# Performance work log

Hardware: AMD Instinct MI355X
Metric: run time of the kernel (lower is better)

## Reference

```python
import jax, jax.numpy as jnp
import numpy as np

N_MEL = 80


def _bce_with_logits(x, t):
    # mean over all elements, numerically stable
    return jnp.mean(jnp.maximum(x, 0.0) - x * t + jnp.log1p(jnp.exp(-jnp.abs(x))))


def _spectral_mel_loss(pred, target):
    w = np.ones(N_MEL, dtype=np.float32)
    w[N_MEL // 4: 3 * N_MEL // 4] *= 1.5
    w[3 * N_MEL // 4:] *= 0.8
    w = jnp.asarray(w)[None, :, None]
    weighted_mse = jnp.mean((pred * w - target * w) ** 2)
    l1 = jnp.mean(jnp.abs(pred - target))
    dp = pred[:, :, 1:] - pred[:, :, :-1]
    dt = target[:, :, 1:] - target[:, :, :-1]
    spectral = jnp.mean((dp - dt) ** 2)
    return weighted_mse + 0.3 * l1 + 0.2 * spectral


def _perceptual_loss(pred, target):
    fw = jnp.exp(-jnp.arange(N_MEL, dtype=jnp.float32) / 20.0)[None, :, None]
    weighted = ((pred - target) ** 2) * fw
    l1 = jnp.mean(jnp.abs(pred - target))
    return jnp.mean(weighted) + 0.5 * l1


def _style_loss(pred, target):
    mean_loss = jnp.mean((jnp.mean(pred, axis=2) - jnp.mean(target, axis=2)) ** 2)
    # torch.var defaults to unbiased (ddof=1)
    var_loss = jnp.mean((jnp.var(pred, axis=2, ddof=1) - jnp.var(target, axis=2, ddof=1)) ** 2)
    c, t = pred.shape[1], pred.shape[2]
    gram_p = jnp.einsum('bct,bdt->bcd', pred, pred) / (c * t)
    gram_t = jnp.einsum('bct,bdt->bcd', target, target) / (c * t)
    gram_loss = jnp.mean((gram_p - gram_t) ** 2)
    return mean_loss + var_loss + 0.5 * gram_loss


def _monotonic_loss(att):
    # att: [B, mel_len, text_len]; vectorized form of the per-step violation loop
    b, mel_len, _ = att.shape
    peaks = jnp.argmax(att, axis=2).astype(jnp.float32)  # [B, mel_len]
    viol = jnp.maximum(peaks[:, :-1] - peaks[:, 1:], 0.0)
    return jnp.sum(viol) / (b * mel_len)


def setup_inputs() -> dict:
    key = jax.random.key(0)
    ks = jax.random.split(key, 6)
    B, C, T, L = 64, N_MEL, 2000, 200
    return {
        'mel_out': jax.random.normal(ks[0], (B, C, T), jnp.float32),
        'mel_out_postnet': jax.random.normal(ks[1], (B, C, T), jnp.float32),
        'mel_target': jax.random.normal(ks[2], (B, C, T), jnp.float32),
        'gate_out': jax.random.normal(ks[3], (B, T), jnp.float32),
        'gate_target': jax.random.uniform(ks[4], (B, T), jnp.float32),
        'attention_weights': jax.random.uniform(ks[5], (B, T, L), jnp.float32),
    }


def reference(mel_out, mel_out_postnet, mel_target, gate_out, gate_target, attention_weights):
    # loss weights (hparams defaults); guide_loss omitted (method truncated in source)
    mel_w, gate_w, spec_w, perc_w, style_w, mono_w = 1.0, 1.0, 0.3, 0.2, 0.1, 0.1
    gate_inner_w = 1.3  # AdaptiveGateLoss initial_weight

    mel_loss = jnp.mean((mel_out - mel_target) ** 2) + jnp.mean((mel_out_postnet - mel_target) ** 2)
    gate_loss = gate_inner_w * _bce_with_logits(gate_out.reshape(-1, 1), gate_target.reshape(-1, 1))
    spectral = _spectral_mel_loss(mel_out_postnet, mel_target)
    perceptual = _perceptual_loss(mel_out_postnet, mel_target)
    style = _style_loss(mel_out_postnet, mel_target)
    mono = _monotonic_loss(attention_weights)

    total = (mel_w * mel_loss + gate_w * gate_loss + spec_w * spectral
             + perc_w * perceptual + style_w * style + mono_w * mono)
    return total
```

## Files before the change

kernel.cpp:

```cpp
#include <hip/hip_runtime.h>
#include <math.h>

#define N_MEL 80
#define B_    64
#define T_    2000
#define L_    200
#define ROWS   (B_*N_MEL)
#define NTOT   (B_*N_MEL*T_)
#define GATE_N (B_*T_)
#define ATT_ROWS (B_*T_)
#define AV_ROWS 64
#define NVIOL  (ATT_ROWS/AV_ROWS)

#define G_MELROW 5120
#define G_GRAM   512
#define G_ARGV   NVIOL
#define G_GATE   64

#define WS_ROWPART 0
#define WS_M8      (WS_ROWPART + ROWS*8)
#define WS_GATEP   (WS_M8 + 8*64*6400)
#define WS_VIOLP   (WS_GATEP + 64)
#define WS_GFP     (WS_VIOLP + NVIOL)

typedef __attribute__((ext_vector_type(8)))  short bf16x8;
typedef __attribute__((ext_vector_type(16))) float f32x16;
typedef unsigned short ush;

__device__ __forceinline__ float blockReduceSum256(float v) {
    __shared__ float red[4];
    #pragma unroll
    for (int off = 32; off; off >>= 1) v += __shfl_down(v, off, 64);
    int lane = threadIdx.x & 63, w = threadIdx.x >> 6;
    if (lane == 0) red[w] = v;
    __syncthreads();
    if (threadIdx.x == 0) v = red[0] + red[1] + red[2] + red[3];
    return v;
}

__device__ __forceinline__ unsigned short f2bf(float f) {
    unsigned u = __float_as_uint(f);
    u = (u + 0x7fffu + ((u >> 16) & 1u)) >> 16;
    return (unsigned short)u;
}

__device__ __forceinline__ void scan_sub(const float* __restrict__ rowp, int q,
                                         float& bOut, int& pOut) {
    const float4* rp = (const float4*)rowp;
    float bx=-1.f, by=-1.f, bz=-1.f, bw=-1.f;
    int jx=0, jy=0, jz=0, jw=0;
    const int n = (q < 2) ? 13 : 12;
    #pragma unroll
    for (int i = 0; i < 13; i++) {
        if (i < n) {
            int j = q + 4*i;
            float4 v = rp[j];
            if (v.x > bx) { bx = v.x; jx = j; }
            if (v.y > by) { by = v.y; jy = j; }
            if (v.z > bz) { bz = v.z; jz = j; }
            if (v.w > bw) { bw = v.w; jw = j; }
        }
    }
    float b = bx; int p = 4*jx;
    if (by > b || (by == b && 4*jy+1 < p)) { b = by; p = 4*jy+1; }
    if (bz > b || (bz == b && 4*jz+2 < p)) { b = bz; p = 4*jz+2; }
    if (bw > b || (bw == b && 4*jw+3 < p)) { b = bw; p = 4*jw+3; }
    bOut = b; pOut = p;
}

__device__ __forceinline__ void merge4(float& b, int& p) {
    #pragma unroll
    for (int m = 1; m <= 2; m <<= 1) {
        float ob = __shfl_xor(b, m, 64);
        int   op = __shfl_xor(p, m, 64);
        if (ob > b || (ob == b && op < p)) { b = ob; p = op; }
    }
}

__global__ __launch_bounds__(256) void k_mega(const float* __restrict__ mo,
                                              const float* __restrict__ mp,
                                              const float* __restrict__ mt,
                                              const float* __restrict__ gx,
                                              const float* __restrict__ gt,
                                              const float* __restrict__ att,
                                              float* __restrict__ ws) {
    __shared__ alignas(16) unsigned char smem[18432];
    const int bid = blockIdx.x;
    float* rowpart = ws + WS_ROWPART;
    float* M8      = ws + WS_M8;
    float* gatep   = ws + WS_GATEP;
    float* violp   = ws + WS_VIOLP;

    if (bid < G_MELROW) {
        const int row = bid;
        const long base = (long)row * T_;
        const float4* mo4 = (const float4*)(mo + base);
        const float4* mp4 = (const float4*)(mp + base);
        const float4* mt4 = (const float4*)(mt + base);

        float s1 = 0, s2 = 0, sl1 = 0, std_ = 0, sp = 0, sp2 = 0, st = 0, st2 = 0;
        for (int i = threadIdx.x; i < T_/4; i += 256) {
            float4 a = mo4[i], p = mp4[i], t = mt4[i];
            float e0 = a.x - t.x, e1 = a.y - t.y, e2 = a.z - t.z, e3 = a.w - t.w;
            s1 += e0*e0 + e1*e1 + e2*e2 + e3*e3;
            float d0 = p.x - t.x, d1 = p.y - t.y, d2 = p.z - t.z, d3 = p.w - t.w;
            s2 += d0*d0 + d1*d1 + d2*d2 + d3*d3;
            sl1 += fabsf(d0) + fabsf(d1) + fabsf(d2) + fabsf(d3);
            sp  += p.x + p.y + p.z + p.w;
            sp2 += p.x*p.x + p.y*p.y + p.z*p.z + p.w*p.w;
            st  += t.x + t.y + t.z + t.w;
            st2 += t.x*t.x + t.y*t.y + t.z*t.z + t.w*t.w;
            float q1 = d1 - d0, q2 = d2 - d1, q3 = d3 - d2;
            std_ += q1*q1 + q2*q2 + q3*q3;
            if (i > 0) {
                float dprev = mp[base + 4*i - 1] - mt[base + 4*i - 1];
                float q0 = d0 - dprev;
                std_ += q0*q0;
            }
        }

        float (*red)[8] = reinterpret_cast<float(*)[8]>(smem);
        float vals[8] = {s1, s2, sl1, std_, sp, sp2, st, st2};
        #pragma unroll
        for (int k = 0; k < 8; k++) {
            float v = vals[k];
            #pragma unroll
            for (int off = 32; off; off >>= 1) v += __shfl_down(v, off, 64);
            vals[k] = v;
        }
        int lane = threadIdx.x & 63, w = threadIdx.x >> 6;
        if (lane == 0) {
            #pragma unroll
            for (int k = 0; k < 8; k++) red[w][k] = vals[k];
        }
        __syncthreads();
        if (threadIdx.x == 0) {
            #pragma unroll
            for (int k = 0; k < 8; k++)
                rowpart[row*8 + k] = red[0][k] + red[1][k] + red[2][k] + red[3][k];
        }
        return;
    }

    if (bid < G_MELROW + G_GRAM) {
        const int gb = bid - G_MELROW;
        const int b  = gb >> 3;
        const int kc = gb & 7;
        const int k0 = kc * 256;
        const int NS = (kc < 7) ? 16 : 13;

        ush (*Dls)[96][24] = reinterpret_cast<ush(*)[96][24]>(smem);
        ush (*Sls)[96][24] = reinterpret_cast<ush(*)[96][24]>(smem + 9216);

        const int tid  = threadIdx.x;
        const bool act = (tid < 192);
        const int row  = tid >> 1;
        const int half = tid & 1;
        const int lane = tid & 63;
        const int wv   = tid >> 6;
        const long bbase = (long)b * (N_MEL * T_);
        const float* prow = mp + bbase + (long)(row < 80 ? row : 0) * T_ + k0 + half * 8;
        const float* trow = mt + bbase + (long)(row < 80 ? row : 0) * T_ + k0 + half * 8;
        const bool rv = act && (row < N_MEL);

        f32x16 acc0 = {}, acc1 = {}, acc2 = {};
        float4 pa0, pa1, ta0, ta1;

        auto loadreg = [&](int s) {
            if (rv) {
                pa0 = *(const float4*)(prow + s*16);
                pa1 = *(const float4*)(prow + s*16 + 4);
                ta0 = *(const float4*)(trow + s*16);
                ta1 = *(const float4*)(trow + s*16 + 4);
            } else {
                pa0 = pa1 = ta0 = ta1 = make_float4(0.f, 0.f, 0.f, 0.f);
            }
        };
        auto writelds = [&](int buf) {
            bf16x8 d, s;
            d[0]=f2bf(pa0.x-ta0.x); d[1]=f2bf(pa0.y-ta0.y); d[2]=f2bf(pa0.z-ta0.z); d[3]=f2bf(pa0.w-ta0.w);
            d[4]=f2bf(pa1.x-ta1.x); d[5]=f2bf(pa1.y-ta1.y); d[6]=f2bf(pa1.z-ta1.z); d[7]=f2bf(pa1.w-ta1.w);
            s[0]=f2bf(pa0.x+ta0.x); s[1]=f2bf(pa0.y+ta0.y); s[2]=f2bf(pa0.z+ta0.z); s[3]=f2bf(pa0.w+ta0.w);
            s[4]=f2bf(pa1.x+ta1.x); s[5]=f2bf(pa1.y+ta1.y); s[6]=f2bf(pa1.z+ta1.z); s[7]=f2bf(pa1.w+ta1.w);
            *(bf16x8*)&Dls[buf][row][half*8] = d;
            *(bf16x8*)&Sls[buf][row][half*8] = s;
        };

        if (act) { loadreg(0); writelds(0); }
        __syncthreads();

        const int frow = lane & 31;
        const int fkh  = lane >> 5;
        for (int s = 0; s < NS; s++) {
            const int cur = s & 1;
            if (act) {
                if (s + 1 < NS) loadreg(s + 1);
                bf16x8 af = *(const bf16x8*)&Dls[cur][wv*32 + frow][fkh*8];
                bf16x8 b0 = *(const bf16x8*)&Sls[cur][      frow][fkh*8];
                bf16x8 b1 = *(const bf16x8*)&Sls[cur][ 32 + frow][fkh*8];
                bf16x8 b2 = *(const bf16x8*)&Sls[cur][ 64 + frow][fkh*8];
                acc0 = __builtin_amdgcn_mfma_f32_32x32x16_bf16(af, b0, acc0, 0, 0, 0);
                acc1 = __builtin_amdgcn_mfma_f32_32x32x16_bf16(af, b1, acc1, 0, 0, 0);
                acc2 = __builtin_amdgcn_mfma_f32_32x32x16_bf16(af, b2, acc2, 0, 0, 0);
                if (s + 1 < NS) writelds((s + 1) & 1);
            }
            __syncthreads();
        }

        if (act) {
            float* Mb = M8 + ((long)(kc * B_ + b)) * 6400;
            #pragma unroll
            for (int r = 0; r < 16; r++) {
                int row32 = (r & 3) + 8 * (r >> 2) + 4 * (lane >> 5);
                int c = wv * 32 + row32;
                if (c < N_MEL) {
                    Mb[c*80 + frow]      = acc0[r];
                    Mb[c*80 + 32 + frow] = acc1[r];
                    if (frow < 16) Mb[c*80 + 64 + frow] = acc2[r];
                }
            }
        }
        return;
    }

    if (bid < G_MELROW + G_GRAM + G_ARGV) {
        const int ab = bid - (G_MELROW + G_GRAM);
        float* pk = reinterpret_cast<float*>(smem);
        const int g = threadIdx.x >> 2;
        const int q = threadIdx.x & 3;
        const int r0 = ab * AV_ROWS;
        const int r  = r0 + g;

        float b; int p;
        scan_sub(att + (long)r * L_, q, b, p);
        merge4(b, p);
        if (q == 0) pk[g] = (float)p;

        const int rb = r0 + AV_ROWS;
        const bool need_b = ((rb % T_) != 0) && (rb < ATT_ROWS);
        if (g == 0 && need_b) {
            float b2; int p2;
            scan_sub(att + (long)rb * L_, q, b2, p2);
            merge4(b2, p2);
            if (q == 0) pk[AV_ROWS] = (float)p2;
        }
        __syncthreads();

        float s = 0;
        if (threadIdx.x < AV_ROWS) {
            int rr = r0 + threadIdx.x;
            if (((rr + 1) % T_) != 0)
                s = fmaxf(pk[threadIdx.x] - pk[threadIdx.x + 1], 0.0f);
        }
        float tot = blockReduceSum256(s);
        if (threadIdx.x == 0) violp[ab] = tot;
        return;
    }

    {
        const int gb = bid - (G_MELROW + G_GRAM + G_ARGV);
        const float4* x4 = (const float4*)gx;
        const float4* t4 = (const float4*)gt;
        float s = 0;
        for (int i = gb*256 + threadIdx.x; i < GATE_N/4; i += G_GATE*256) {
            float4 x = x4[i], t = t4[i];
            float xs[4] = {x.x, x.y, x.z, x.w}, ts[4] = {t.x, t.y, t.z, t.w};
            #pragma unroll
            for (int k = 0; k < 4; k++)
                s += fmaxf(xs[k], 0.0f) - xs[k]*ts[k] + log1pf(expf(-fabsf(xs[k])));
        }
        float tot = blockReduceSum256(s);
        if (threadIdx.x == 0) gatep[gb] = tot;
    }
}

__global__ __launch_bounds__(256) void k_gramfin(const float* __restrict__ ws_ro,
                                                 float* __restrict__ gfp) {
    __shared__ float Ms[N_MEL][N_MEL + 1];
    const float* M8 = ws_ro + WS_M8;
    const int b = blockIdx.x;
    const float inv = 1.0f / (float)(N_MEL * T_);

    for (int i = threadIdx.x; i < 6400; i += 256) {
        float m = 0.f;
        #pragma unroll
        for (int kc = 0; kc < 8; kc++)
            m += M8[((long)(kc * B_ + b)) * 6400 + i];
        Ms[i / N_MEL][i % N_MEL] = m;
    }
    __syncthreads();

    float s = 0.f;
    for (int i = threadIdx.x; i < 6400; i += 256) {
        int c = i / N_MEL, d = i % N_MEL;
        float g = 0.5f * (Ms[c][d] + Ms[d][c]) * inv;
        s += g * g;
    }
    float tot = blockReduceSum256(s);
    if (threadIdx.x == 0) gfp[b] = tot;
}

__global__ __launch_bounds__(256) void k_final2(const float* __restrict__ ws_ro,
                                                float* __restrict__ out) {
    const float* rowpart = ws_ro + WS_ROWPART;
    const float* gatep   = ws_ro + WS_GATEP;
    const float* violp   = ws_ro + WS_VIOLP;
    const float* gfp     = ws_ro + WS_GFP;

    float a[11] = {0,0,0,0,0,0,0,0,0,0,0};
    for (int row = threadIdx.x; row < ROWS; row += 256) {
        const float4 lo = *(const float4*)(rowpart + row*8);
        const float4 hi = *(const float4*)(rowpart + row*8 + 4);
        int c = row % N_MEL;
        float wc = (c >= 3*N_MEL/4) ? 0.8f : ((c >= N_MEL/4) ? 1.5f : 1.0f);
        float fw = expf(-(float)c / 20.0f);
        a[0] += lo.x;
        a[1] += lo.y;
        a[2] += wc*wc*lo.y;
        a[3] += lo.z;
        a[4] += lo.w;
        a[5] += fw*lo.y;
        float md = (hi.x - hi.z) * (1.0f / T_);
        a[6] += md*md;
        float vp = (hi.y - hi.x*hi.x*(1.0f/T_)) * (1.0f/(T_-1));
        float vt = (hi.w - hi.z*hi.z*(1.0f/T_)) * (1.0f/(T_-1));
        float vd = vp - vt;
        a[7] += vd*vd;
    }
    for (int i = threadIdx.x; i < NVIOL; i += 256) a[9] += violp[i];
    if (threadIdx.x < 64) { a[8] = gatep[threadIdx.x]; a[10] = gfp[threadIdx.x]; }

    __shared__ float red[4][11];
    #pragma unroll
    for (int k = 0; k < 11; k++) {
        float v = a[k];
        #pragma unroll
        for (int off = 32; off; off >>= 1) v += __shfl_down(v, off, 64);
        a[k] = v;
    }
    int lane = threadIdx.x & 63, w = threadIdx.x >> 6;
    if (lane == 0) {
        #pragma unroll
        for (int k = 0; k < 11; k++) red[w][k] = a[k];
    }
    __syncthreads();
    if (threadIdx.x == 0) {
        float r[11];
        #pragma unroll
        for (int k = 0; k < 11; k++) r[k] = red[0][k] + red[1][k] + red[2][k] + red[3][k];
        const float invN = 1.0f / (float)NTOT;
        float mel        = (r[0] + r[1]) * invN;
        float gate       = 1.3f * r[8] / (float)GATE_N;
        float wmse       = r[2] * invN;
        float l1         = r[3] * invN;
        float sdiff      = r[4] / (float)(B_ * N_MEL * (T_ - 1));
        float spectral   = wmse + 0.3f*l1 + 0.2f*sdiff;
        float perceptual = r[5]*invN + 0.5f*l1;
        float mean_loss  = r[6] / (float)ROWS;
        float var_loss   = r[7] / (float)ROWS;
        float gram       = r[10] / (float)(B_ * 6400);
        float style      = mean_loss + var_loss + 0.5f*gram;
        float mono       = r[9] / (float)(B_ * T_);
        out[0] = mel + gate + 0.3f*spectral + 0.2f*perceptual + 0.1f*style + 0.1f*mono;
    }
}

extern "C" void kernel_launch(void* const* d_in, const int* in_sizes, int n_in,
                              void* d_out, int out_size, void* d_ws, size_t ws_size,
                              hipStream_t stream) {
    const float* mo  = (const float*)d_in[0];
    const float* mp  = (const float*)d_in[1];
    const float* mt  = (const float*)d_in[2];
    const float* gx  = (const float*)d_in[3];
    const float* gt  = (const float*)d_in[4];
    const float* att = (const float*)d_in[5];
    float* ws = (float*)d_ws;

    const int g1 = G_MELROW + G_GRAM + G_ARGV + G_GATE;
    k_mega   <<<g1, 256, 0, stream>>>(mo, mp, mt, gx, gt, att, ws);
    k_gramfin<<<64, 256, 0, stream>>>(ws, ws + WS_GFP);
    k_final2 <<<1,  256, 0, stream>>>(ws, (float*)d_out);
}
```

Measured before the change: 89.04 us.

## Split gram MFMA work out of mega-kernel into separate 192-thread kernel

Moves the bf16 MFMA gram computation out of the single heterogeneous mega-kernel into its own kernel launched with 192 threads. The streaming kernel now holds only the row, argmax and gate branches with small shared-memory footprints, and it orders argmax blocks first. This is meant to cut LDS and register pressure so the memory-bound streaming blocks get higher occupancy. The cost is an extra launch, and the gram kernel rereads mp/mt after they were already streamed, possibly from cache.

```diff
diff --git a/kernel.cpp b/kernel.cpp
--- a/kernel.cpp
+++ b/kernel.cpp
@@ -12,10 +12,9 @@
 #define AV_ROWS 64
 #define NVIOL  (ATT_ROWS/AV_ROWS)
 
-#define G_MELROW 5120
-#define G_GRAM   512
 #define G_ARGV   NVIOL
 #define G_GATE   64
+#define G_MELROW ROWS
 
 #define WS_ROWPART 0
 #define WS_M8      (WS_ROWPART + ROWS*8)
@@ -77,22 +76,71 @@
     }
 }
 
-__global__ __launch_bounds__(256) void k_mega(const float* __restrict__ mo,
-                                              const float* __restrict__ mp,
-                                              const float* __restrict__ mt,
-                                              const float* __restrict__ gx,
-                                              const float* __restrict__ gt,
-                                              const float* __restrict__ att,
-                                              float* __restrict__ ws) {
-    __shared__ alignas(16) unsigned char smem[18432];
+__global__ __launch_bounds__(256) void k_stream(const float* __restrict__ mo,
+                                                const float* __restrict__ mp,
+                                                const float* __restrict__ mt,
+                                                const float* __restrict__ gx,
+                                                const float* __restrict__ gt,
+                                                const float* __restrict__ att,
+                                                float* __restrict__ ws) {
     const int bid = blockIdx.x;
     float* rowpart = ws + WS_ROWPART;
-    float* M8      = ws + WS_M8;
     float* gatep   = ws + WS_GATEP;
     float* violp   = ws + WS_VIOLP;
 
-    if (bid < G_MELROW) {
-        const int row = bid;
+    if (bid < G_ARGV) {
+        __shared__ float pk[AV_ROWS + 1];
+        const int ab = bid;
+        const int g = threadIdx.x >> 2;
+        const int q = threadIdx.x & 3;
+        const int r0 = ab * AV_ROWS;
+        const int r  = r0 + g;
+
+        float b; int p;
+        scan_sub(att + (long)r * L_, q, b, p);
+        merge4(b, p);
+        if (q == 0) pk[g] = (float)p;
+
+        const int rb = r0 + AV_ROWS;
+        const bool need_b = ((rb % T_) != 0) && (rb < ATT_ROWS);
+        if (g == 0 && need_b) {
+            float b2; int p2;
+            scan_sub(att + (long)rb * L_, q, b2, p2);
+            merge4(b2, p2);
+            if (q == 0) pk[AV_ROWS] = (float)p2;
+        }
+        __syncthreads();
+
+        float s = 0;
+        if (threadIdx.x < AV_ROWS) {
+            int rr = r0 + threadIdx.x;
+            if (((rr + 1) % T_) != 0)
+                s = fmaxf(pk[threadIdx.x] - pk[threadIdx.x + 1], 0.0f);
+        }
+        float tot = blockReduceSum256(s);
+        if (threadIdx.x == 0) violp[ab] = tot;
+        return;
+    }
+
+    if (bid < G_ARGV + G_GATE) {
+        const int gb = bid - G_ARGV;
+        const float4* x4 = (const float4*)gx;
+        const float4* t4 = (const float4*)gt;
+        float s = 0;
+        for (int i = gb*256 + threadIdx.x; i < GATE_N/4; i += G_GATE*256) {
+            float4 x = x4[i], t = t4[i];
+            float xs[4] = {x.x, x.y, x.z, x.w}, ts[4] = {t.x, t.y, t.z, t.w};
+            #pragma unroll
+            for (int k = 0; k < 4; k++)
+                s += fmaxf(xs[k], 0.0f) - xs[k]*ts[k] + log1pf(expf(-fabsf(xs[k])));
+        }
+        float tot = blockReduceSum256(s);
+        if (threadIdx.x == 0) gatep[gb] = tot;
+        return;
+    }
+
+    {
+        const int row = bid - (G_ARGV + G_GATE);
         const long base = (long)row * T_;
         const float4* mo4 = (const float4*)(mo + base);
         const float4* mp4 = (const float4*)(mp + base);
@@ -119,7 +167,7 @@
             }
         }
 
-        float (*red)[8] = reinterpret_cast<float(*)[8]>(smem);
+        __shared__ float red8[4][8];
         float vals[8] = {s1, s2, sl1, std_, sp, sp2, st, st2};
         #pragma unroll
         for (int k = 0; k < 8; k++) {
@@ -131,146 +179,91 @@
         int lane = threadIdx.x & 63, w = threadIdx.x >> 6;
         if (lane == 0) {
             #pragma unroll
-            for (int k = 0; k < 8; k++) red[w][k] = vals[k];
+            for (int k = 0; k < 8; k++) red8[w][k] = vals[k];
         }
         __syncthreads();
         if (threadIdx.x == 0) {
             #pragma unroll
             for (int k = 0; k < 8; k++)
-                rowpart[row*8 + k] = red[0][k] + red[1][k] + red[2][k] + red[3][k];
-        }
-        return;
-    }
-
-    if (bid < G_MELROW + G_GRAM) {
-        const int gb = bid - G_MELROW;
-        const int b  = gb >> 3;
-        const int kc = gb & 7;
-        const int k0 = kc * 256;
-        const int NS = (kc < 7) ? 16 : 13;
-
-        ush (*Dls)[96][24] = reinterpret_cast<ush(*)[96][24]>(smem);
-        ush (*Sls)[96][24] = reinterpret_cast<ush(*)[96][24]>(smem + 9216);
-
-        const int tid  = threadIdx.x;
-        const bool act = (tid < 192);
-        const int row  = tid >> 1;
-        const int half = tid & 1;
-        const int lane = tid & 63;
-        const int wv   = tid >> 6;
-        const long bbase = (long)b * (N_MEL * T_);
-        const float* prow = mp + bbase + (long)(row < 80 ? row : 0) * T_ + k0 + half * 8;
-        const float* trow = mt + bbase + (long)(row < 80 ? row : 0) * T_ + k0 + half * 8;
-        const bool rv = act && (row < N_MEL);
-
-        f32x16 acc0 = {}, acc1 = {}, acc2 = {};
-        float4 pa0, pa1, ta0, ta1;
-
-        auto loadreg = [&](int s) {
-            if (rv) {
-                pa0 = *(const float4*)(prow + s*16);
-                pa1 = *(const float4*)(prow + s*16 + 4);
-                ta0 = *(const float4*)(trow + s*16);
-                ta1 = *(const float4*)(trow + s*16 + 4);
-            } else {
-                pa0 = pa1 = ta0 = ta1 = make_float4(0.f, 0.f, 0.f, 0.f);
-            }
-        };
-        auto writelds = [&](int buf) {
-            bf16x8 d, s;
-            d[0]=f2bf(pa0.x-ta0.x); d[1]=f2bf(pa0.y-ta0.y); d[2]=f2bf(pa0.z-ta0.z); d[3]=f2bf(pa0.w-ta0.w);
-            d[4]=f2bf(pa1.x-ta1.x); d[5]=f2bf(pa1.y-ta1.y); d[6]=f2bf(pa1.z-ta1.z); d[7]=f2bf(pa1.w-ta1.w);
-            s[0]=f2bf(pa0.x+ta0.x); s[1]=f2bf(pa0.y+ta0.y); s[2]=f2bf(pa0.z+ta0.z); s[3]=f2bf(pa0.w+ta0.w);
-            s[4]=f2bf(pa1.x+ta1.x); s[5]=f2bf(pa1.y+ta1.y); s[6]=f2bf(pa1.z+ta1.z); s[7]=f2bf(pa1.w+ta1.w);
-            *(bf16x8*)&Dls[buf][row][half*8] = d;
-            *(bf16x8*)&Sls[buf][row][half*8] = s;
-        };
-
-        if (act) { loadreg(0); writelds(0); }
+                rowpart[row*8 + k] = red8[0][k] + red8[1][k] + red8[2][k] + red8[3][k];
+        }
+    }
+}
+
+__global__ __launch_bounds__(192) void k_gram(const float* __restrict__ mp,
+                                              const float* __restrict__ mt,
+                                              float* __restrict__ M8) {
+    const int b  = blockIdx.x >> 3;
+    const int kc = blockIdx.x & 7;
+    const int k0 = kc * 256;
+    const int NS = (kc < 7) ? 16 : 13;
+
+    __shared__ ush Dls[2][96][24];
+    __shared__ ush Sls[2][96][24];
+
+    const int tid  = threadIdx.x;
+    const int row  = tid >> 1;
+    const int half = tid & 1;
+    const int lane = tid & 63;
+    const int wv   = tid >> 6;
+    const long bbase = (long)b * (N_MEL * T_);
+    const float* prow = mp + bbase + (long)row * T_ + k0 + half * 8;
+    const float* trow = mt + bbase + (long)row * T_ + k0 + half * 8;
+    const bool rv = (row < N_MEL);
+
+    f32x16 acc0 = {}, acc1 = {}, acc2 = {};
+    float4 pa0, pa1, ta0, ta1;
+
+    auto loadreg = [&](int s) {
+        if (rv) {
+            pa0 = *(const float4*)(prow + s*16);
+            pa1 = *(const float4*)(prow + s*16 + 4);
+            ta0 = *(const float4*)(trow + s*16);
+            ta1 = *(const float4*)(trow + s*16 + 4);
+        } else {
+            pa0 = pa1 = ta0 = ta1 = make_float4(0.f, 0.f, 0.f, 0.f);
+        }
+    };
+    auto writelds = [&](int buf) {
+        bf16x8 d, s;
+        d[0]=f2bf(pa0.x-ta0.x); d[1]=f2bf(pa0.y-ta0.y); d[2]=f2bf(pa0.z-ta0.z); d[3]=f2bf(pa0.w-ta0.w);
+        d[4]=f2bf(pa1.x-ta1.x); d[5]=f2bf(pa1.y-ta1.y); d[6]=f2bf(pa1.z-ta1.z); d[7]=f2bf(pa1.w-ta1.w);
+        s[0]=f2bf(pa0.x+ta0.x); s[1]=f2bf(pa0.y+ta0.y); s[2]=f2bf(pa0.z+ta0.z); s[3]=f2bf(pa0.w+ta0.w);
+        s[4]=f2bf(pa1.x+ta1.x); s[5]=f2bf(pa1.y+ta1.y); s[6]=f2bf(pa1.z+ta1.z); s[7]=f2bf(pa1.w+ta1.w);
+        *(bf16x8*)&Dls[buf][row][half*8] = d;
+        *(bf16x8*)&Sls[buf][row][half*8] = s;
+    };
+
+    loadreg(0);
+    writelds(0);
+    __syncthreads();
+
+    const int frow = lane & 31;
+    const int fkh  = lane >> 5;
+    for (int s = 0; s < NS; s++) {
+        const int cur = s & 1;
+        if (s + 1 < NS) loadreg(s + 1);
+        bf16x8 af = *(const bf16x8*)&Dls[cur][wv*32 + frow][fkh*8];
+        bf16x8 b0 = *(const bf16x8*)&Sls[cur][      frow][fkh*8];
+        bf16x8 b1 = *(const bf16x8*)&Sls[cur][ 32 + frow][fkh*8];
+        bf16x8 b2 = *(const bf16x8*)&Sls[cur][ 64 + frow][fkh*8];
+        acc0 = __builtin_amdgcn_mfma_f32_32x32x16_bf16(af, b0, acc0, 0, 0, 0);
+        acc1 = __builtin_amdgcn_mfma_f32_32x32x16_bf16(af, b1, acc1, 0, 0, 0);
+        acc2 = __builtin_amdgcn_mfma_f32_32x32x16_bf16(af, b2, acc2, 0, 0, 0);
+        if (s + 1 < NS) writelds((s + 1) & 1);
         __syncthreads();
-
-        const int frow = lane & 31;
-        const int fkh  = lane >> 5;
-        for (int s = 0; s < NS; s++) {
-            const int cur = s & 1;
-            if (act) {
-                if (s + 1 < NS) loadreg(s + 1);
-                bf16x8 af = *(const bf16x8*)&Dls[cur][wv*32 + frow][fkh*8];
-                bf16x8 b0 = *(const bf16x8*)&Sls[cur][      frow][fkh*8];
-                bf16x8 b1 = *(const bf16x8*)&Sls[cur][ 32 + frow][fkh*8];
-                bf16x8 b2 = *(const bf16x8*)&Sls[cur][ 64 + frow][fkh*8];
-                acc0 = __builtin_amdgcn_mfma_f32_32x32x16_bf16(af, b0, acc0, 0, 0, 0);
-                acc1 = __builtin_amdgcn_mfma_f32_32x32x16_bf16(af, b1, acc1, 0, 0, 0);
-                acc2 = __builtin_amdgcn_mfma_f32_32x32x16_bf16(af, b2, acc2, 0, 0, 0);
-                if (s + 1 < NS) writelds((s + 1) & 1);
-            }
-            __syncthreads();
-        }
-
-        if (act) {
-            float* Mb = M8 + ((long)(kc * B_ + b)) * 6400;
-            #pragma unroll
-            for (int r = 0; r < 16; r++) {
-                int row32 = (r & 3) + 8 * (r >> 2) + 4 * (lane >> 5);
-                int c = wv * 32 + row32;
-                if (c < N_MEL) {
-                    Mb[c*80 + frow]      = acc0[r];
-                    Mb[c*80 + 32 + frow] = acc1[r];
-                    if (frow < 16) Mb[c*80 + 64 + frow] = acc2[r];
-                }
-            }
-        }
-        return;
-    }
-
-    if (bid < G_MELROW + G_GRAM + G_ARGV) {
-        const int ab = bid - (G_MELROW + G_GRAM);
-        float* pk = reinterpret_cast<float*>(smem);
-        const int g = threadIdx.x >> 2;
-        const int q = threadIdx.x & 3;
-        const int r0 = ab * AV_ROWS;
-        const int r  = r0 + g;
-
-        float b; int p;
-        scan_sub(att + (long)r * L_, q, b, p);
-        merge4(b, p);
-        if (q == 0) pk[g] = (float)p;
-
-        const int rb = r0 + AV_ROWS;
-        const bool need_b = ((rb % T_) != 0) && (rb < ATT_ROWS);
-        if (g == 0 && need_b) {
-            float b2; int p2;
-            scan_sub(att + (long)rb * L_, q, b2, p2);
-            merge4(b2, p2);
-            if (q == 0) pk[AV_ROWS] = (float)p2;
-        }
-        __syncthreads();
-
-        float s = 0;
-        if (threadIdx.x < AV_ROWS) {
-            int rr = r0 + threadIdx.x;
-            if (((rr + 1) % T_) != 0)
-                s = fmaxf(pk[threadIdx.x] - pk[threadIdx.x + 1], 0.0f);
-        }
-        float tot = blockReduceSum256(s);
-        if (threadIdx.x == 0) violp[ab] = tot;
-        return;
-    }
-
-    {
-        const int gb = bid - (G_MELROW + G_GRAM + G_ARGV);
-        const float4* x4 = (const float4*)gx;
-        const float4* t4 = (const float4*)gt;
-        float s = 0;
-        for (int i = gb*256 + threadIdx.x; i < GATE_N/4; i += G_GATE*256) {
-            float4 x = x4[i], t = t4[i];
-            float xs[4] = {x.x, x.y, x.z, x.w}, ts[4] = {t.x, t.y, t.z, t.w};
-            #pragma unroll
-            for (int k = 0; k < 4; k++)
-                s += fmaxf(xs[k], 0.0f) - xs[k]*ts[k] + log1pf(expf(-fabsf(xs[k])));
-        }
-        float tot = blockReduceSum256(s);
-        if (threadIdx.x == 0) gatep[gb] = tot;
+    }
+
+    float* Mb = M8 + ((long)(kc * B_ + b)) * 6400;
+    #pragma unroll
+    for (int r = 0; r < 16; r++) {
+        int row32 = (r & 3) + 8 * (r >> 2) + 4 * (lane >> 5);
+        int c = wv * 32 + row32;
+        if (c < N_MEL) {
+            Mb[c*80 + frow]      = acc0[r];
+            Mb[c*80 + 32 + frow] = acc1[r];
+            if (frow < 16) Mb[c*80 + 64 + frow] = acc2[r];
+        }
     }
 }
 
@@ -376,8 +369,9 @@
     const float* att = (const float*)d_in[5];
     float* ws = (float*)d_ws;
 
-    const int g1 = G_MELROW + G_GRAM + G_ARGV + G_GATE;
-    k_mega   <<<g1, 256, 0, stream>>>(mo, mp, mt, gx, gt, att, ws);
-    k_gramfin<<<64, 256, 0, stream>>>(ws, ws + WS_GFP);
-    k_final2 <<<1,  256, 0, stream>>>(ws, (float*)d_out);
-}
+    const int g1 = G_ARGV + G_GATE + G_MELROW;
+    k_stream <<<g1,  256, 0, stream>>>(mo, mp, mt, gx, gt, att, ws);
+    k_gram   <<<512, 192, 0, stream>>>(mp, mt, ws + WS_M8);
+    k_gramfin<<<64,  256, 0, stream>>>(ws, ws + WS_GFP);
+    k_final2 <<<1,   256, 0, stream>>>(ws, (float*)d_out);
+}
```

After: 90.60 us. No clear change (+1.7%).
